# Performance work log

Hardware: AMD Instinct MI355X
Metric: run time of the kernel (lower is better)

## Reference

```python
import jax, jax.numpy as jnp
import numpy as np

TOP_K = 2


def setup_inputs() -> dict:
    key = jax.random.key(0)
    k1, k2, k3, k4 = jax.random.split(key, 4)
    B, T, C, E = 4, 4096, 4096, 4
    return {
        "hidden_states": jax.random.normal(k1, (B, T, C), dtype=jnp.float32),
        "mass": jax.random.uniform(k2, (B, T, 1), dtype=jnp.float32),
        "gate_w": jax.random.normal(k3, (E, C), dtype=jnp.float32) * (1.0 / np.sqrt(C)),
        "mass_bias": jax.random.normal(k4, (E,), dtype=jnp.float32) * 0.02,
    }


def reference(hidden_states, mass, gate_w, mass_bias):
    B, T, C = hidden_states.shape
    E = gate_w.shape[0]
    flat_hidden = hidden_states.reshape(-1, C)          # [N, C], N = B*T
    flat_mass = mass.reshape(-1, 1)                     # [N, 1]
    # gate: Linear without bias -> x @ W^T
    logits = jnp.einsum("nc,ec->ne", flat_hidden, gate_w)
    logits = logits + flat_mass * mass_bias[None, :]    # physics impact
    probs = jax.nn.softmax(logits, axis=-1)
    top_k_weights, top_k_indices = jax.lax.top_k(probs, TOP_K)
    expert_importance = probs.sum(axis=0)               # [E]
    target_load = probs.shape[0] / E
    aux_loss = jnp.mean((expert_importance - target_load) ** 2)
    return logits, top_k_indices, aux_loss, top_k_weights
```

## Files before the change

kernel.cpp:

```cpp
#include <hip/hip_runtime.h>


#define NEXP 4
#define ROWS_PER_WAVE 2

__global__ __launch_bounds__(256, 4) void physics_router_main(
    const float* __restrict__ hidden,
    const float* __restrict__ mass,
    const float* __restrict__ gate,
    const float* __restrict__ bias,
    float* __restrict__ out_logits,
    float* __restrict__ out_idx,
    float* __restrict__ out_w,
    float* __restrict__ ws_sums,
    int C)
{
    __shared__ float lds_sum[NEXP];
    const int tid = threadIdx.x;
    if (tid < NEXP) lds_sum[tid] = 0.f;
    __syncthreads();

    const int lane = tid & 63;
    const int wave_in_block = tid >> 6;
    const int gwave = blockIdx.x * 4 + wave_in_block;
    const int n0 = gwave * ROWS_PER_WAVE;

    float acc[ROWS_PER_WAVE][NEXP];
#pragma unroll
    for (int r = 0; r < ROWS_PER_WAVE; ++r)
#pragma unroll
        for (int e = 0; e < NEXP; ++e) acc[r][e] = 0.f;

    const float4* __restrict__ gate4 = reinterpret_cast<const float4*>(gate);
    const float4* __restrict__ hid4  = reinterpret_cast<const float4*>(hidden);
    const int C4 = C >> 2;
    const int steps = C >> 9;

    for (int it = 0; it < steps; ++it) {
        const int c4 = (it << 7) + lane;
        float4 g0[NEXP], g1[NEXP];
#pragma unroll
        for (int e = 0; e < NEXP; ++e) {
            g0[e] = gate4[(size_t)e * C4 + c4];
            g1[e] = gate4[(size_t)e * C4 + c4 + 64];
        }
        float4 h0[ROWS_PER_WAVE], h1[ROWS_PER_WAVE];
#pragma unroll
        for (int r = 0; r < ROWS_PER_WAVE; ++r) {
            h0[r] = hid4[(size_t)(n0 + r) * C4 + c4];
            h1[r] = hid4[(size_t)(n0 + r) * C4 + c4 + 64];
        }
#pragma unroll
        for (int r = 0; r < ROWS_PER_WAVE; ++r) {
#pragma unroll
            for (int e = 0; e < NEXP; ++e) {
                float a = acc[r][e];
                a = fmaf(h0[r].x, g0[e].x, a);
                a = fmaf(h0[r].y, g0[e].y, a);
                a = fmaf(h0[r].z, g0[e].z, a);
                a = fmaf(h0[r].w, g0[e].w, a);
                a = fmaf(h1[r].x, g1[e].x, a);
                a = fmaf(h1[r].y, g1[e].y, a);
                a = fmaf(h1[r].z, g1[e].z, a);
                a = fmaf(h1[r].w, g1[e].w, a);
                acc[r][e] = a;
            }
        }
    }

#pragma unroll
    for (int r = 0; r < ROWS_PER_WAVE; ++r)
#pragma unroll
        for (int e = 0; e < NEXP; ++e) {
            float v = acc[r][e];
#pragma unroll
            for (int off = 32; off >= 1; off >>= 1)
                v += __shfl_xor(v, off, 64);
            acc[r][e] = v;
        }

    if (lane < ROWS_PER_WAVE) {
        const int n = n0 + lane;
        const float m = mass[n];
        float l[NEXP];
#pragma unroll
        for (int e = 0; e < NEXP; ++e) l[e] = acc[lane][e] + m * bias[e];

        reinterpret_cast<float4*>(out_logits)[n] =
            make_float4(l[0], l[1], l[2], l[3]);

        const float mx = fmaxf(fmaxf(l[0], l[1]), fmaxf(l[2], l[3]));
        float p[NEXP];
        float s = 0.f;
#pragma unroll
        for (int e = 0; e < NEXP; ++e) { p[e] = __expf(l[e] - mx); s += p[e]; }
        const float inv = __frcp_rn(s);
#pragma unroll
        for (int e = 0; e < NEXP; ++e) p[e] *= inv;

        int i0 = 0;
#pragma unroll
        for (int e = 1; e < NEXP; ++e) if (p[e] > p[i0]) i0 = e;
        int i1 = (i0 == 0) ? 1 : 0;
#pragma unroll
        for (int e = 0; e < NEXP; ++e)
            if (e != i0 && p[e] > p[i1]) i1 = e;

        out_idx[2 * n]     = (float)i0;
        out_idx[2 * n + 1] = (float)i1;
        out_w[2 * n]       = p[i0];
        out_w[2 * n + 1]   = p[i1];

#pragma unroll
        for (int e = 0; e < NEXP; ++e) atomicAdd(&lds_sum[e], p[e]);
    }
    __syncthreads();
    if (tid < NEXP) atomicAdd(&ws_sums[tid], lds_sum[tid]);
}

__global__ void physics_router_aux(const float* __restrict__ ws_sums,
                                   float* __restrict__ out_aux,
                                   float target)
{
    if (threadIdx.x == 0) {
        float a = 0.f;
#pragma unroll
        for (int e = 0; e < NEXP; ++e) {
            const float d = ws_sums[e] - target;
            a += d * d;
        }
        out_aux[0] = a * (1.f / NEXP);
    }
}

extern "C" void kernel_launch(void* const* d_in, const int* in_sizes, int n_in,
                              void* d_out, int out_size, void* d_ws, size_t ws_size,
                              hipStream_t stream) {
    const float* hidden = (const float*)d_in[0];
    const float* mass   = (const float*)d_in[1];
    const float* gate   = (const float*)d_in[2];
    const float* bias   = (const float*)d_in[3];

    const int N = in_sizes[1];
    const int E = in_sizes[3];
    const int C = in_sizes[2] / E;

    float* out = (float*)d_out;
    float* out_logits = out;
    float* out_idx    = out + (size_t)N * 4;
    float* out_aux    = out + (size_t)N * 6;
    float* out_w      = out + (size_t)N * 6 + 1;

    float* ws_sums = (float*)d_ws;
    hipMemsetAsync(ws_sums, 0, NEXP * sizeof(float), stream);

    const int rows_per_block = 4 * ROWS_PER_WAVE;
    const int grid = (N + rows_per_block - 1) / rows_per_block;
    physics_router_main<<<grid, 256, 0, stream>>>(
        hidden, mass, gate, bias, out_logits, out_idx, out_w, ws_sums, C);

    const float target = (float)N / (float)E;
    physics_router_aux<<<1, 64, 0, stream>>>(ws_sums, out_aux, target);
}
```

Before: 369.6 us.

## Stage gate weights in LDS and process four rows per wave with 512-thread blocks

Each block now copies the whole 64KB gate matrix into shared memory and reads it from LDS instead of global/L2 in the inner loop. Each wave handles four rows instead of two, and blocks grow to 512 threads, so each gate load is reused across more rows. C is hardcoded to 4096, so the kernel only works for that hidden size. The 64KB LDS per block limits how many blocks fit per CU, and every block pays for the gate copy up front.

Result: no change. 373.2 us (+1.0%).

```diff
diff --git a/kernel.cpp b/kernel.cpp
--- a/kernel.cpp
+++ b/kernel.cpp
@@ -2,9 +2,9 @@
 
 
 #define NEXP 4
-#define ROWS_PER_WAVE 2
+#define RPW 4
 
-__global__ __launch_bounds__(256, 4) void physics_router_main(
+__global__ __launch_bounds__(512, 4) void physics_router_main(
     const float* __restrict__ hidden,
     const float* __restrict__ mass,
     const float* __restrict__ gate,
@@ -12,46 +12,49 @@
     float* __restrict__ out_logits,
     float* __restrict__ out_idx,
     float* __restrict__ out_w,
-    float* __restrict__ ws_sums,
-    int C)
+    float* __restrict__ ws_sums)
 {
+    __shared__ float4 gsh[NEXP * 1024];
     __shared__ float lds_sum[NEXP];
+
     const int tid = threadIdx.x;
     if (tid < NEXP) lds_sum[tid] = 0.f;
+
+    const float4* __restrict__ gate4 = reinterpret_cast<const float4*>(gate);
+#pragma unroll
+    for (int i = 0; i < 8; ++i)
+        gsh[tid + i * 512] = gate4[tid + i * 512];
     __syncthreads();
 
     const int lane = tid & 63;
-    const int wave_in_block = tid >> 6;
-    const int gwave = blockIdx.x * 4 + wave_in_block;
-    const int n0 = gwave * ROWS_PER_WAVE;
+    const int wid  = tid >> 6;
+    const int n0   = (blockIdx.x * 8 + wid) * RPW;
 
-    float acc[ROWS_PER_WAVE][NEXP];
+    float acc[RPW][NEXP];
 #pragma unroll
-    for (int r = 0; r < ROWS_PER_WAVE; ++r)
+    for (int r = 0; r < RPW; ++r)
 #pragma unroll
         for (int e = 0; e < NEXP; ++e) acc[r][e] = 0.f;
 
-    const float4* __restrict__ gate4 = reinterpret_cast<const float4*>(gate);
-    const float4* __restrict__ hid4  = reinterpret_cast<const float4*>(hidden);
-    const int C4 = C >> 2;
-    const int steps = C >> 9;
+    const float4* __restrict__ hid4 = reinterpret_cast<const float4*>(hidden);
 
-    for (int it = 0; it < steps; ++it) {
+#pragma unroll 2
+    for (int it = 0; it < 8; ++it) {
         const int c4 = (it << 7) + lane;
+        float4 h0[RPW], h1[RPW];
+#pragma unroll
+        for (int r = 0; r < RPW; ++r) {
+            h0[r] = hid4[(size_t)(n0 + r) * 1024 + c4];
+            h1[r] = hid4[(size_t)(n0 + r) * 1024 + c4 + 64];
+        }
         float4 g0[NEXP], g1[NEXP];
 #pragma unroll
         for (int e = 0; e < NEXP; ++e) {
-            g0[e] = gate4[(size_t)e * C4 + c4];
-            g1[e] = gate4[(size_t)e * C4 + c4 + 64];
-        }
-        float4 h0[ROWS_PER_WAVE], h1[ROWS_PER_WAVE];
-#pragma unroll
-        for (int r = 0; r < ROWS_PER_WAVE; ++r) {
-            h0[r] = hid4[(size_t)(n0 + r) * C4 + c4];
-            h1[r] = hid4[(size_t)(n0 + r) * C4 + c4 + 64];
+            g0[e] = gsh[e * 1024 + c4];
+            g1[e] = gsh[e * 1024 + c4 + 64];
         }
 #pragma unroll
-        for (int r = 0; r < ROWS_PER_WAVE; ++r) {
+        for (int r = 0; r < RPW; ++r) {
 #pragma unroll
             for (int e = 0; e < NEXP; ++e) {
                 float a = acc[r][e];
@@ -69,7 +72,7 @@
     }
 
 #pragma unroll
-    for (int r = 0; r < ROWS_PER_WAVE; ++r)
+    for (int r = 0; r < RPW; ++r)
 #pragma unroll
         for (int e = 0; e < NEXP; ++e) {
             float v = acc[r][e];
@@ -79,7 +82,7 @@
             acc[r][e] = v;
         }
 
-    if (lane < ROWS_PER_WAVE) {
+    if (lane < RPW) {
         const int n = n0 + lane;
         const float m = mass[n];
         float l[NEXP];
@@ -143,7 +146,6 @@
 
     const int N = in_sizes[1];
     const int E = in_sizes[3];
-    const int C = in_sizes[2] / E;
 
     float* out = (float*)d_out;
     float* out_logits = out;
@@ -154,10 +156,10 @@
     float* ws_sums = (float*)d_ws;
     hipMemsetAsync(ws_sums, 0, NEXP * sizeof(float), stream);
 
-    const int rows_per_block = 4 * ROWS_PER_WAVE;
+    const int rows_per_block = 8 * RPW;
     const int grid = (N + rows_per_block - 1) / rows_per_block;
-    physics_router_main<<<grid, 256, 0, stream>>>(
-        hidden, mass, gate, bias, out_logits, out_idx, out_w, ws_sums, C);
+    physics_router_main<<<grid, 512, 0, stream>>>(
+        hidden, mass, gate, bias, out_logits, out_idx, out_w, ws_sums);
 
     const float target = (float)N / (float)E;
     physics_router_aux<<<1, 64, 0, stream>>>(ws_sums, out_aux, target);
```
